# Performance work log

Hardware: AMD Instinct MI355X
Metric: run time of the kernel (lower is better)

Reference implementation:

```python
import jax, jax.numpy as jnp
import numpy as np

SR = 16000
NFFT = 512
HOP = 256
NMELS = 64
NFREQ = NFFT // 2 + 1  # 257
BATCH = 32
WAVE_LEN = 960000  # 60 s at 16 kHz


def _mel_matrix():
    # librosa.filters.mel(sr=16000, n_fft=512, n_mels=64, fmin=20, fmax=8000, htk=True, norm=None).T
    def hz2mel(f):
        return 2595.0 * np.log10(1.0 + np.asarray(f, dtype=np.float64) / 700.0)

    def mel2hz(m):
        return 700.0 * (10.0 ** (np.asarray(m, dtype=np.float64) / 2595.0) - 1.0)

    mel_pts = np.linspace(hz2mel(20.0), hz2mel(8000.0), NMELS + 2)
    hz_pts = mel2hz(mel_pts)                      # [n_mels+2]
    fft_freqs = np.linspace(0.0, SR / 2.0, NFREQ)  # [257]
    fdiff = np.diff(hz_pts)
    ramps = hz_pts[:, None] - fft_freqs[None, :]
    lower = -ramps[:-2] / fdiff[:-1, None]
    upper = ramps[2:] / fdiff[1:, None]
    w = np.maximum(0.0, np.minimum(lower, upper))  # [n_mels, 257], norm=None
    return jnp.asarray(w.T.astype(np.float32))     # [257, n_mels]


def _stft_mag(x):
    # torch-stft style: reflect-pad by n_fft//2, hann window (periodic), hop=256
    pad = NFFT // 2
    xp = jnp.pad(x, ((0, 0), (pad, pad)), mode='reflect')  # [B, L+2*pad]
    n_frames = (xp.shape[1] - NFFT) // HOP + 1
    idx = np.arange(n_frames)[:, None] * HOP + np.arange(NFFT)[None, :]  # [T, NFFT]
    frames = xp[:, idx]  # [B, T, NFFT]
    win = (0.5 - 0.5 * np.cos(2.0 * np.pi * np.arange(NFFT) / NFFT)).astype(np.float32)
    spec = jnp.fft.rfft(frames * win, axis=-1)  # [B, T, 257] complex
    re, im = jnp.real(spec), jnp.imag(spec)
    return jnp.sqrt(re * re + im * im)  # (spec**2).sum(-1).sqrt()


def setup_inputs() -> dict:
    key = jax.random.key(0)
    wav = jax.random.normal(key, (BATCH, WAVE_LEN), dtype=jnp.float32)
    alpha = jnp.full((1, NFREQ), 3.0, dtype=jnp.float32)  # nn.init.constant_(self.alpha, 3)
    return {"input_waveform": wav, "alpha": alpha, "mel_matrix": _mel_matrix()}


def reference(input_waveform, alpha, mel_matrix):
    mag = _stft_mag(input_waveform)          # [B, T, F]
    a = jax.nn.sigmoid(alpha)[0]             # [F]

    # EMA recurrence: tmp = a*tmp + (1-a)*mag[:, i], tmp0 = mag[:, 0]
    def step(carry, x_t):
        c = a * carry + (1.0 - a) * x_t
        return c, c

    mag_t = jnp.moveaxis(mag, 1, 0)          # [T, B, F] time-major for scan
    _, avg_t = jax.lax.scan(step, mag[:, 0, :], mag_t)
    avg_mag = jnp.moveaxis(avg_t, 0, 1)      # [B, T, F]

    norm_mag = mag / (avg_mag + 1e-8)
    abs_mel = jnp.matmul(norm_mag, mel_matrix) + 1e-6  # [B, T, n_mels]
    return abs_mel
```

## Files before the change

kernel.cpp:

```cpp
#include <hip/hip_runtime.h>
#include <math.h>

#define NFFT      512
#define HOP       256
#define NBINS     257
#define NMELS     64
#define BATCH     32
#define WAVE_LEN  960000
#define NFRAMES   3751
#define NPAIRS    1876
#define CHUNK     64
#define NCHUNK    59
#define MROWS     (BATCH * NFRAMES)
#define KPAD      288
#define LDSW      296

#define PI2F 6.283185307179586f

typedef unsigned short ushort_t;
typedef __attribute__((ext_vector_type(2))) float f32x2;
typedef __attribute__((ext_vector_type(8))) short bf16x8;
typedef __attribute__((ext_vector_type(4))) float f32x4;

__device__ __forceinline__ float sigmoidf_(float x) { return 1.0f / (1.0f + __expf(-x)); }

__device__ __forceinline__ ushort_t f2b(float x) {
  unsigned u = __float_as_uint(x);
  u = u + 0x7FFFu + ((u >> 16) & 1u);
  return (ushort_t)(u >> 16);
}
__device__ __forceinline__ float b2f(ushort_t h) {
  return __uint_as_float(((unsigned)h) << 16);
}

__global__ __launch_bounds__(512) void init_tables(const float* __restrict__ mel,
                                                   float* __restrict__ win,
                                                   float* __restrict__ twA,
                                                   float* __restrict__ twB,
                                                   ushort_t* __restrict__ melbT) {
  const int n = threadIdx.x;
  win[n] = 0.5f - 0.5f * __cosf(PI2F * (float)n / (float)NFFT);
  {
    int j = n >> 6, p = n & 63;
    float ang = -PI2F * (float)(p * j) / 512.0f;
    twA[2 * n]     = __cosf(ang);
    twA[2 * n + 1] = __sinf(ang);
  }
  if (n < 64) {
    int p = n >> 3, j = n & 7;
    float ang = -PI2F * (float)(p * j) / 64.0f;
    twB[2 * n]     = __cosf(ang);
    twB[2 * n + 1] = __sinf(ang);
  }
  for (int i = n; i < NMELS * KPAD; i += 512) {
    int m = i / KPAD, k = i - m * KPAD;
    melbT[i] = (k < NBINS) ? f2b(mel[(size_t)k * NMELS + m]) : (ushort_t)0;
  }
}

__device__ __forceinline__ f32x2 cmulw(f32x2 a, float c, float s) {
  return (f32x2){a.x * c - a.y * s, a.y * c + a.x * s};
}

__device__ __forceinline__ void fft8v(f32x2 z[8]) {
  f32x2 e[4], o[4];
  {
    f32x2 A = z[0] + z[4], C = z[0] - z[4];
    f32x2 B = z[2] + z[6], D = z[2] - z[6];
    f32x2 Dn = (f32x2){D.y, -D.x};
    e[0] = A + B; e[2] = A - B; e[1] = C + Dn; e[3] = C - Dn;
  }
  {
    f32x2 A = z[1] + z[5], C = z[1] - z[5];
    f32x2 B = z[3] + z[7], D = z[3] - z[7];
    f32x2 Dn = (f32x2){D.y, -D.x};
    o[0] = A + B; o[2] = A - B; o[1] = C + Dn; o[3] = C - Dn;
  }
  const float R = 0.70710678118654752f;
  z[0] = e[0] + o[0]; z[4] = e[0] - o[0];
  f32x2 t1 = (f32x2){R * (o[1].x + o[1].y), R * (o[1].y - o[1].x)};
  z[1] = e[1] + t1; z[5] = e[1] - t1;
  f32x2 t2 = (f32x2){o[2].y, -o[2].x};
  z[2] = e[2] + t2; z[6] = e[2] - t2;
  f32x2 t3 = (f32x2){R * (o[3].y - o[3].x), -R * (o[3].x + o[3].y)};
  z[3] = e[3] + t3; z[7] = e[3] - t3;
}

__global__ __launch_bounds__(64) void stft_kernel(const float* __restrict__ wav,
                                                  const float* __restrict__ win,
                                                  const float* __restrict__ twA,
                                                  const float* __restrict__ twB,
                                                  ushort_t* __restrict__ mag) {
  const int pr  = blockIdx.x;
  const int b   = blockIdx.y;
  const int tid = threadIdx.x;

  __shared__ f32x2 sz[576];

  const float* w = wav + (size_t)b * WAVE_LEN;
  const int f0 = 2 * pr, f1 = f0 + 1;
  const bool has1 = (f1 < NFRAMES);
  const int base0 = f0 * HOP - (NFFT / 2);
  const int base1 = base0 + HOP;

  f32x2 z[8];
#pragma unroll
  for (int j = 0; j < 8; ++j) {
    int n = tid + 64 * j;
    float wn = win[n];
    int p0 = base0 + n;
    p0 = (p0 < 0) ? -p0 : p0;
    p0 = (p0 >= WAVE_LEN) ? (2 * WAVE_LEN - 2 - p0) : p0;
    float x0 = w[p0];
    float x1 = has1 ? w[base1 + n] : 0.0f;
    z[j] = (f32x2){x0 * wn, x1 * wn};
  }

  fft8v(z);
  const float2* twA2 = (const float2*)twA;
#pragma unroll
  for (int j = 1; j < 8; ++j) {
    float2 t = twA2[j * 64 + tid];
    z[j] = cmulw(z[j], t.x, t.y);
  }

#pragma unroll
  for (int j = 0; j < 8; ++j) {
    int n = tid + 64 * j;
    sz[n + (n >> 3)] = z[j];
  }
  __syncthreads();
  const int g = tid >> 3, q = tid & 7;
#pragma unroll
  for (int j = 0; j < 8; ++j) {
    int n = g * 64 + q + 8 * j;
    z[j] = sz[n + (n >> 3)];
  }

  fft8v(z);
  const float2* twB2 = (const float2*)twB;
#pragma unroll
  for (int j = 1; j < 8; ++j) {
    float2 t = twB2[q * 8 + j];
    z[j] = cmulw(z[j], t.x, t.y);
  }

  __syncthreads();
#pragma unroll
  for (int j = 0; j < 8; ++j) {
    int n = g * 64 + q + 8 * j;
    sz[n + (n >> 3)] = z[j];
  }
  __syncthreads();
#pragma unroll
  for (int j = 0; j < 8; ++j) {
    z[j] = sz[9 * tid + j];
  }

  fft8v(z);

  __syncthreads();
#pragma unroll
  for (int j = 0; j < 8; ++j) {
    int k = 64 * j + 8 * q + g;
    sz[k] = z[j];
  }
  __syncthreads();

  ushort_t* out0 = mag + ((size_t)b * NFRAMES + f0) * NBINS;
  ushort_t* out1 = out0 + NBINS;
  for (int k = tid; k <= 256; k += 64) {
    int kn = (NFFT - k) & (NFFT - 1);
    f32x2 A = sz[k], B = sz[kn];
    float xr = A.x + B.x, xi = A.y - B.y;
    float yr = A.y + B.y, yi = A.x - B.x;
    out0[k] = f2b(0.5f * sqrtf(xr * xr + xi * xi));
    if (has1) out1[k] = f2b(0.5f * sqrtf(yr * yr + yi * yi));
  }
}

__global__ void scan_partial(const ushort_t* __restrict__ mag,
                             const float* __restrict__ alpha,
                             float* __restrict__ Bc) {
  const int c = blockIdx.x, b = blockIdx.y, f = threadIdx.x;
  if (f >= NBINS) return;
  const float a = sigmoidf_(alpha[f]);
  const float om = 1.0f - a;
  const int t0 = c * CHUNK;
  const int t1 = min(NFRAMES, t0 + CHUNK);
  const ushort_t* p = mag + ((size_t)b * NFRAMES + t0) * NBINS + f;
  float v = 0.0f;
  for (int t = t0; t < t1; ++t) {
    v = fmaf(a, v, om * b2f(*p));
    p += NBINS;
  }
  Bc[((size_t)b * NBINS + f) * NCHUNK + c] = v;
}

__global__ void scan_combine(const ushort_t* __restrict__ mag,
                             const float* __restrict__ alpha,
                             const float* __restrict__ Bc,
                             float* __restrict__ carry) {
  const int b = blockIdx.x, f = threadIdx.x;
  if (f >= NBINS) return;
  const float a = sigmoidf_(alpha[f]);
  float aL = a;
#pragma unroll
  for (int i = 0; i < 6; ++i) aL *= aL;
  float v = b2f(mag[(size_t)b * NFRAMES * NBINS + f]);
  const size_t off = ((size_t)b * NBINS + f) * NCHUNK;
  for (int c = 0; c < NCHUNK; ++c) {
    carry[off + c] = v;
    v = fmaf(aL, v, Bc[off + c]);
  }
}

__global__ __launch_bounds__(256) void scan_gemm(const ushort_t* __restrict__ magb,
                                                 const float* __restrict__ alpha,
                                                 const float* __restrict__ carry,
                                                 const ushort_t* __restrict__ melbT,
                                                 float* __restrict__ out) {
  const int c = blockIdx.x, b = blockIdx.y;
  const int tid = threadIdx.x;
  const int t0 = c * CHUNK;
  const int nv = min(CHUNK, NFRAMES - t0);

  __shared__ __align__(16) ushort_t Ns[CHUNK][LDSW];

  for (int f = tid; f < KPAD; f += 256) {
    if (f < NBINS) {
      const float a = sigmoidf_(alpha[f]);
      const float om = 1.0f - a;
      float v = carry[((size_t)b * NBINS + f) * NCHUNK + c];
      const ushort_t* p = magb + ((size_t)b * NFRAMES + t0) * NBINS + f;
      int t = 0;
      for (; t < nv; ++t) {
        float m = b2f(*p);
        v = fmaf(a, v, om * m);
        Ns[t][f] = f2b(m / (v + 1e-8f));
        p += NBINS;
      }
      for (; t < CHUNK; ++t) Ns[t][f] = 0;
    } else {
      for (int t = 0; t < CHUNK; ++t) Ns[t][f] = 0;
    }
  }
  __syncthreads();

  const int wave = tid >> 6, lane = tid & 63;
  const int m = lane & 15, quad = lane >> 4;
  const int r0 = wave * 16;

  f32x4 acc[4];
#pragma unroll
  for (int ct = 0; ct < 4; ++ct) acc[ct] = (f32x4){0.f, 0.f, 0.f, 0.f};

#pragma unroll
  for (int ks = 0; ks < 9; ++ks) {
    bf16x8 a = *(const bf16x8*)&Ns[r0 + m][ks * 32 + quad * 8];
#pragma unroll
    for (int ct = 0; ct < 4; ++ct) {
      bf16x8 bb = *(const bf16x8*)(melbT + (size_t)(ct * 16 + m) * KPAD + ks * 32 + quad * 8);
      acc[ct] = __builtin_amdgcn_mfma_f32_16x16x32_bf16(a, bb, acc[ct], 0, 0, 0);
    }
  }

#pragma unroll
  for (int ct = 0; ct < 4; ++ct) {
#pragma unroll
    for (int r = 0; r < 4; ++r) {
      int tl = r0 + quad * 4 + r;
      if (t0 + tl < NFRAMES)
        out[((size_t)b * NFRAMES + t0 + tl) * NMELS + ct * 16 + m] = acc[ct][r] + 1e-6f;
    }
  }
}

extern "C" void kernel_launch(void* const* d_in, const int* in_sizes, int n_in,
                              void* d_out, int out_size, void* d_ws, size_t ws_size,
                              hipStream_t stream) {
  const float* wav   = (const float*)d_in[0];
  const float* alpha = (const float*)d_in[1];
  const float* mel   = (const float*)d_in[2];
  float* out = (float*)d_out;

  ushort_t* magb  = (ushort_t*)d_ws;
  ushort_t* melbT = magb + (size_t)BATCH * NFRAMES * NBINS;
  float* Bc    = (float*)(melbT + (size_t)NMELS * KPAD);
  float* carry = Bc + (size_t)BATCH * NBINS * NCHUNK;
  float* win   = carry + (size_t)BATCH * NBINS * NCHUNK;
  float* twA   = win + 512;
  float* twB   = twA + 1024;

  init_tables<<<1, 512, 0, stream>>>(mel, win, twA, twB, melbT);
  stft_kernel<<<dim3(NPAIRS, BATCH), 64, 0, stream>>>(wav, win, twA, twB, magb);
  scan_partial<<<dim3(NCHUNK, BATCH), 320, 0, stream>>>(magb, alpha, Bc);
  scan_combine<<<BATCH, 320, 0, stream>>>(magb, alpha, Bc, carry);
  scan_gemm<<<dim3(NCHUNK, BATCH), 256, 0, stream>>>(magb, alpha, carry, melbT, out);
}
```

Measured before the change: 315.5 us.

## Fuse STFT with per-chunk scan partials and process four frame pairs per block

The STFT kernel now processes four frame pairs per block and computes the EMA chunk partial sums in-register from the freshly rounded magnitudes. This removes the separate scan_partial pass that re-read the whole magnitude buffer. Twiddles, window and alpha are hoisted into registers, LDS is split into separate real/imag arrays, and an interior fast path skips the reflect-index math. The scan chunk size drops to 8 frames, so scan_combine runs a longer serial loop (469 steps), and the division in scan_gemm is replaced by a hardware reciprocal, which is slightly less accurate.

```diff
diff --git a/kernel.cpp b/kernel.cpp
--- a/kernel.cpp
+++ b/kernel.cpp
@@ -9,8 +9,10 @@
 #define WAVE_LEN  960000
 #define NFRAMES   3751
 #define NPAIRS    1876
-#define CHUNK     64
-#define NCHUNK    59
+#define CH1       8
+#define NCH1      469
+#define CHG       64
+#define NCHG      59
 #define MROWS     (BATCH * NFRAMES)
 #define KPAD      288
 #define LDSW      296
@@ -86,115 +88,156 @@
   z[3] = e[3] + t3; z[7] = e[3] - t3;
 }
 
-__global__ __launch_bounds__(64) void stft_kernel(const float* __restrict__ wav,
-                                                  const float* __restrict__ win,
-                                                  const float* __restrict__ twA,
-                                                  const float* __restrict__ twB,
-                                                  ushort_t* __restrict__ mag) {
-  const int pr  = blockIdx.x;
+__global__ __launch_bounds__(64) void stft_scan(const float* __restrict__ wav,
+                                                const float* __restrict__ win,
+                                                const float* __restrict__ twA,
+                                                const float* __restrict__ twB,
+                                                const float* __restrict__ alpha,
+                                                ushort_t* __restrict__ mag,
+                                                float* __restrict__ Bc) {
+  const int u   = blockIdx.x;
   const int b   = blockIdx.y;
   const int tid = threadIdx.x;
-
-  __shared__ f32x2 sz[576];
+  const int g = tid >> 3, q = tid & 7;
+
+  __shared__ float sre[576], sim[576];
+
+  const float2* twA2 = (const float2*)twA;
+  const float2* twB2 = (const float2*)twB;
+  float2 tA[7], tB[7];
+#pragma unroll
+  for (int j = 1; j < 8; ++j) tA[j - 1] = twA2[j * 64 + tid];
+#pragma unroll
+  for (int j = 1; j < 8; ++j) tB[j - 1] = twB2[q * 8 + j];
+  float wv[8];
+#pragma unroll
+  for (int j = 0; j < 8; ++j) wv[j] = win[tid + 64 * j];
+
+  float av[5], omv[5];
+#pragma unroll
+  for (int i = 0; i < 4; ++i) {
+    float a = sigmoidf_(alpha[tid + 64 * i]);
+    av[i] = a; omv[i] = 1.0f - a;
+  }
+  {
+    float a = sigmoidf_(alpha[256]);
+    av[4] = a; omv[4] = 1.0f - a;
+  }
+  float v[5] = {0.f, 0.f, 0.f, 0.f, 0.f};
 
   const float* w = wav + (size_t)b * WAVE_LEN;
-  const int f0 = 2 * pr, f1 = f0 + 1;
-  const bool has1 = (f1 < NFRAMES);
-  const int base0 = f0 * HOP - (NFFT / 2);
-  const int base1 = base0 + HOP;
-
-  f32x2 z[8];
-#pragma unroll
-  for (int j = 0; j < 8; ++j) {
-    int n = tid + 64 * j;
-    float wn = win[n];
-    int p0 = base0 + n;
-    p0 = (p0 < 0) ? -p0 : p0;
-    p0 = (p0 >= WAVE_LEN) ? (2 * WAVE_LEN - 2 - p0) : p0;
-    float x0 = w[p0];
-    float x1 = has1 ? w[base1 + n] : 0.0f;
-    z[j] = (f32x2){x0 * wn, x1 * wn};
-  }
-
-  fft8v(z);
-  const float2* twA2 = (const float2*)twA;
-#pragma unroll
-  for (int j = 1; j < 8; ++j) {
-    float2 t = twA2[j * 64 + tid];
-    z[j] = cmulw(z[j], t.x, t.y);
-  }
-
-#pragma unroll
-  for (int j = 0; j < 8; ++j) {
-    int n = tid + 64 * j;
-    sz[n + (n >> 3)] = z[j];
-  }
-  __syncthreads();
-  const int g = tid >> 3, q = tid & 7;
-#pragma unroll
-  for (int j = 0; j < 8; ++j) {
-    int n = g * 64 + q + 8 * j;
-    z[j] = sz[n + (n >> 3)];
-  }
-
-  fft8v(z);
-  const float2* twB2 = (const float2*)twB;
-#pragma unroll
-  for (int j = 1; j < 8; ++j) {
-    float2 t = twB2[q * 8 + j];
-    z[j] = cmulw(z[j], t.x, t.y);
-  }
-
-  __syncthreads();
-#pragma unroll
-  for (int j = 0; j < 8; ++j) {
-    int n = g * 64 + q + 8 * j;
-    sz[n + (n >> 3)] = z[j];
-  }
-  __syncthreads();
-#pragma unroll
-  for (int j = 0; j < 8; ++j) {
-    z[j] = sz[9 * tid + j];
-  }
-
-  fft8v(z);
-
-  __syncthreads();
-#pragma unroll
-  for (int j = 0; j < 8; ++j) {
-    int k = 64 * j + 8 * q + g;
-    sz[k] = z[j];
-  }
-  __syncthreads();
-
-  ushort_t* out0 = mag + ((size_t)b * NFRAMES + f0) * NBINS;
-  ushort_t* out1 = out0 + NBINS;
-  for (int k = tid; k <= 256; k += 64) {
-    int kn = (NFFT - k) & (NFFT - 1);
-    f32x2 A = sz[k], B = sz[kn];
-    float xr = A.x + B.x, xi = A.y - B.y;
-    float yr = A.y + B.y, yi = A.x - B.x;
-    out0[k] = f2b(0.5f * sqrtf(xr * xr + xi * xi));
-    if (has1) out1[k] = f2b(0.5f * sqrtf(yr * yr + yi * yi));
-  }
-}
-
-__global__ void scan_partial(const ushort_t* __restrict__ mag,
-                             const float* __restrict__ alpha,
-                             float* __restrict__ Bc) {
-  const int c = blockIdx.x, b = blockIdx.y, f = threadIdx.x;
-  if (f >= NBINS) return;
-  const float a = sigmoidf_(alpha[f]);
-  const float om = 1.0f - a;
-  const int t0 = c * CHUNK;
-  const int t1 = min(NFRAMES, t0 + CHUNK);
-  const ushort_t* p = mag + ((size_t)b * NFRAMES + t0) * NBINS + f;
-  float v = 0.0f;
-  for (int t = t0; t < t1; ++t) {
-    v = fmaf(a, v, om * b2f(*p));
-    p += NBINS;
-  }
-  Bc[((size_t)b * NBINS + f) * NCHUNK + c] = v;
+
+  for (int pi = 0; pi < 4; ++pi) {
+    const int pr = 4 * u + pi;
+    const int f0 = 2 * pr, f1 = f0 + 1;
+    const bool has1 = (f1 < NFRAMES);
+    const int base0 = f0 * HOP - (NFFT / 2);
+    const int base1 = base0 + HOP;
+
+    f32x2 z[8];
+    if (base0 >= 0 && base0 + NFFT <= WAVE_LEN) {
+#pragma unroll
+      for (int j = 0; j < 8; ++j) {
+        int n = tid + 64 * j;
+        float x0 = w[base0 + n];
+        float x1 = has1 ? w[base1 + n] : 0.0f;
+        z[j] = (f32x2){x0 * wv[j], x1 * wv[j]};
+      }
+    } else {
+#pragma unroll
+      for (int j = 0; j < 8; ++j) {
+        int n = tid + 64 * j;
+        int p0 = base0 + n;
+        p0 = (p0 < 0) ? -p0 : p0;
+        p0 = (p0 >= WAVE_LEN) ? (2 * WAVE_LEN - 2 - p0) : p0;
+        float x0 = w[p0];
+        float x1 = has1 ? w[base1 + n] : 0.0f;
+        z[j] = (f32x2){x0 * wv[j], x1 * wv[j]};
+      }
+    }
+
+    fft8v(z);
+#pragma unroll
+    for (int j = 1; j < 8; ++j) z[j] = cmulw(z[j], tA[j - 1].x, tA[j - 1].y);
+
+#pragma unroll
+    for (int j = 0; j < 8; ++j) {
+      int n = tid + 64 * j;
+      int a = n + (n >> 3);
+      sre[a] = z[j].x; sim[a] = z[j].y;
+    }
+    __syncthreads();
+#pragma unroll
+    for (int j = 0; j < 8; ++j) {
+      int n = g * 64 + q + 8 * j;
+      int a = n + (n >> 3);
+      z[j] = (f32x2){sre[a], sim[a]};
+    }
+
+    fft8v(z);
+#pragma unroll
+    for (int j = 1; j < 8; ++j) z[j] = cmulw(z[j], tB[j - 1].x, tB[j - 1].y);
+
+    __syncthreads();
+#pragma unroll
+    for (int j = 0; j < 8; ++j) {
+      int n = g * 64 + q + 8 * j;
+      int a = n + (n >> 3);
+      sre[a] = z[j].x; sim[a] = z[j].y;
+    }
+    __syncthreads();
+#pragma unroll
+    for (int j = 0; j < 8; ++j) {
+      int a = 9 * tid + j;
+      z[j] = (f32x2){sre[a], sim[a]};
+    }
+
+    fft8v(z);
+
+    __syncthreads();
+#pragma unroll
+    for (int j = 0; j < 8; ++j) {
+      int k = 64 * j + 8 * q + g;
+      sre[k] = z[j].x; sim[k] = z[j].y;
+    }
+    __syncthreads();
+
+    ushort_t* out0 = mag + ((size_t)b * NFRAMES + f0) * NBINS;
+    ushort_t* out1 = out0 + NBINS;
+#pragma unroll
+    for (int i = 0; i < 4; ++i) {
+      int k = tid + 64 * i;
+      int kn = (NFFT - k) & (NFFT - 1);
+      float ar = sre[k],  ai = sim[k];
+      float br = sre[kn], bi = sim[kn];
+      float xr = ar + br, xi = ai - bi;
+      float yr = ai + bi, yi = ar - br;
+      ushort_t h0 = f2b(0.5f * __builtin_amdgcn_sqrtf(xr * xr + xi * xi));
+      ushort_t h1 = f2b(0.5f * __builtin_amdgcn_sqrtf(yr * yr + yi * yi));
+      out0[k] = h0;
+      v[i] = fmaf(av[i], v[i], omv[i] * b2f(h0));
+      if (has1) {
+        out1[k] = h1;
+        v[i] = fmaf(av[i], v[i], omv[i] * b2f(h1));
+      }
+    }
+    {
+      ushort_t h0 = f2b(fabsf(sre[256]));
+      ushort_t h1 = f2b(fabsf(sim[256]));
+      if (tid == 0) out0[256] = h0;
+      v[4] = fmaf(av[4], v[4], omv[4] * b2f(h0));
+      if (has1) {
+        if (tid == 0) out1[256] = h1;
+        v[4] = fmaf(av[4], v[4], omv[4] * b2f(h1));
+      }
+    }
+    __syncthreads();
+  }
+
+  float* bco = Bc + ((size_t)b * NCH1 + u) * NBINS;
+#pragma unroll
+  for (int i = 0; i < 4; ++i) bco[tid + 64 * i] = v[i];
+  if (tid == 0) bco[256] = v[4];
 }
 
 __global__ void scan_combine(const ushort_t* __restrict__ mag,
@@ -206,12 +249,15 @@
   const float a = sigmoidf_(alpha[f]);
   float aL = a;
 #pragma unroll
-  for (int i = 0; i < 6; ++i) aL *= aL;
+  for (int i = 0; i < 3; ++i) aL *= aL;
   float v = b2f(mag[(size_t)b * NFRAMES * NBINS + f]);
-  const size_t off = ((size_t)b * NBINS + f) * NCHUNK;
-  for (int c = 0; c < NCHUNK; ++c) {
-    carry[off + c] = v;
-    v = fmaf(aL, v, Bc[off + c]);
+  const float* bcp = Bc + (size_t)b * NCH1 * NBINS + f;
+  float* cp = carry + (size_t)b * NCH1 * NBINS + f;
+  for (int c = 0; c < NCH1; ++c) {
+    *cp = v;
+    v = fmaf(aL, v, *bcp);
+    bcp += NBINS;
+    cp += NBINS;
   }
 }
 
@@ -222,27 +268,28 @@
                                                  float* __restrict__ out) {
   const int c = blockIdx.x, b = blockIdx.y;
   const int tid = threadIdx.x;
-  const int t0 = c * CHUNK;
-  const int nv = min(CHUNK, NFRAMES - t0);
-
-  __shared__ __align__(16) ushort_t Ns[CHUNK][LDSW];
-
+  const int t0 = c * CHG;
+  const int nv = min(CHG, NFRAMES - t0);
+
+  __shared__ __align__(16) ushort_t Ns[CHG][LDSW];
+
+  const float* crow = carry + ((size_t)b * NCH1 + 8 * c) * NBINS;
   for (int f = tid; f < KPAD; f += 256) {
     if (f < NBINS) {
       const float a = sigmoidf_(alpha[f]);
       const float om = 1.0f - a;
-      float v = carry[((size_t)b * NBINS + f) * NCHUNK + c];
+      float v = crow[f];
       const ushort_t* p = magb + ((size_t)b * NFRAMES + t0) * NBINS + f;
       int t = 0;
       for (; t < nv; ++t) {
         float m = b2f(*p);
         v = fmaf(a, v, om * m);
-        Ns[t][f] = f2b(m / (v + 1e-8f));
+        Ns[t][f] = f2b(m * __builtin_amdgcn_rcpf(v + 1e-8f));
         p += NBINS;
       }
-      for (; t < CHUNK; ++t) Ns[t][f] = 0;
+      for (; t < CHG; ++t) Ns[t][f] = 0;
     } else {
-      for (int t = 0; t < CHUNK; ++t) Ns[t][f] = 0;
+      for (int t = 0; t < CHG; ++t) Ns[t][f] = 0;
     }
   }
   __syncthreads();
@@ -287,14 +334,13 @@
   ushort_t* magb  = (ushort_t*)d_ws;
   ushort_t* melbT = magb + (size_t)BATCH * NFRAMES * NBINS;
   float* Bc    = (float*)(melbT + (size_t)NMELS * KPAD);
-  float* carry = Bc + (size_t)BATCH * NBINS * NCHUNK;
-  float* win   = carry + (size_t)BATCH * NBINS * NCHUNK;
+  float* carry = Bc + (size_t)BATCH * NCH1 * NBINS;
+  float* win   = carry + (size_t)BATCH * NCH1 * NBINS;
   float* twA   = win + 512;
   float* twB   = twA + 1024;
 
   init_tables<<<1, 512, 0, stream>>>(mel, win, twA, twB, melbT);
-  stft_kernel<<<dim3(NPAIRS, BATCH), 64, 0, stream>>>(wav, win, twA, twB, magb);
-  scan_partial<<<dim3(NCHUNK, BATCH), 320, 0, stream>>>(magb, alpha, Bc);
+  stft_scan<<<dim3(NCH1, BATCH), 64, 0, stream>>>(wav, win, twA, twB, alpha, magb, Bc);
   scan_combine<<<BATCH, 320, 0, stream>>>(magb, alpha, Bc, carry);
-  scan_gemm<<<dim3(NCHUNK, BATCH), 256, 0, stream>>>(magb, alpha, carry, melbT, out);
-}
+  scan_gemm<<<dim3(NCHG, BATCH), 256, 0, stream>>>(magb, alpha, carry, melbT, out);
+}
```

After: 306.8 us. 1.03x faster.
